# Kernel optimization log

Measured on AMD Instinct MI355X. Metric: run time of the kernel, lower is better.

## Reference

```python
import jax, jax.numpy as jnp
import numpy as np

STATE_DIM = 64
HIDDEN = 128
ACTION_DIM = 10
T = 512
B = 512


def _lstm_cell(x_t, h, c, Wi, Wh, bi, bh):
    # PyTorch LSTMCell: gates ordered (i, f, g, o)
    gates = x_t @ Wi.T + bi + h @ Wh.T + bh  # [B, 4H]
    i, f, g, o = jnp.split(gates, 4, axis=-1)
    c2 = jax.nn.sigmoid(f) * c + jax.nn.sigmoid(i) * jnp.tanh(g)
    h2 = jax.nn.sigmoid(o) * jnp.tanh(c2)
    return h2, c2


def setup_inputs() -> dict:
    key = jax.random.key(0)
    ks = jax.random.split(key, 8)
    x = jax.random.normal(ks[0], (T, B, STATE_DIM), dtype=jnp.float32)
    # LSTMCell params (PyTorch layout: weight_ih [4H, in], weight_hh [4H, H])
    s = 1.0 / np.sqrt(HIDDEN)
    W_ih0 = jax.random.uniform(ks[1], (4 * HIDDEN, STATE_DIM), minval=-s, maxval=s)
    W_hh0 = jax.random.uniform(ks[2], (4 * HIDDEN, HIDDEN), minval=-s, maxval=s)
    b_ih0 = jnp.zeros((4 * HIDDEN,), jnp.float32)
    b_hh0 = jnp.zeros((4 * HIDDEN,), jnp.float32)
    W_ih1 = jax.random.uniform(ks[3], (4 * HIDDEN, HIDDEN), minval=-s, maxval=s)
    W_hh1 = jax.random.uniform(ks[4], (4 * HIDDEN, HIDDEN), minval=-s, maxval=s)
    b_ih1 = jnp.zeros((4 * HIDDEN,), jnp.float32)
    b_hh1 = jnp.zeros((4 * HIDDEN,), jnp.float32)
    # output Linear, normc init per normc_fn
    W_out = jax.random.normal(ks[5], (ACTION_DIM, HIDDEN), dtype=jnp.float32)
    W_out = W_out / jnp.sqrt(jnp.sum(W_out ** 2, axis=1, keepdims=True))
    b_out = jnp.zeros((ACTION_DIM,), jnp.float32)
    return {"x": x, "W_ih0": W_ih0, "W_hh0": W_hh0, "b_ih0": b_ih0, "b_hh0": b_hh0,
            "W_ih1": W_ih1, "W_hh1": W_hh1, "b_ih1": b_ih1, "b_hh1": b_hh1,
            "W_out": W_out, "b_out": b_out}


def reference(x, W_ih0, W_hh0, b_ih0, b_hh0, W_ih1, W_hh1, b_ih1, b_hh1, W_out, b_out):
    # x: [T, B, state_dim]. 3D branch of LSTM_model.forward: fresh zero state,
    # two stacked LSTM cells unrolled over time, then action = tanh(Linear(h_all)).
    batch = x.shape[1]
    h0 = jnp.zeros((batch, HIDDEN), x.dtype)
    init = (h0, h0, h0, h0)  # (h_l0, c_l0, h_l1, c_l1)

    def step(carry, x_t):
        h0_, c0_, h1_, c1_ = carry
        h0n, c0n = _lstm_cell(x_t, h0_, c0_, W_ih0, W_hh0, b_ih0, b_hh0)
        h1n, c1n = _lstm_cell(h0n, h1_, c1_, W_ih1, W_hh1, b_ih1, b_hh1)
        return (h0n, c0n, h1n, c1n), h1n

    _, y = jax.lax.scan(step, init, x)  # y: [T, B, HIDDEN]
    action = jnp.tanh(y @ W_out.T + b_out)  # [T, B, action_dim]
    return action
```

## Files before the change

### kernel.cpp

```cpp
#include <hip/hip_runtime.h>
#include <stdint.h>

#define T_STEPS 512
#define B_ALL   512
#define SDIM    64
#define HID     128
#define ADIM    10
#define CB      16
#define NCH     32
#define LROW    17
#define SROW    129
#define WPAD    132

typedef __attribute__((ext_vector_type(4))) float f32x4;
typedef __attribute__((ext_vector_type(8))) short s16x8;

#define MFMA(a,b,c) __builtin_amdgcn_mfma_f32_16x16x32_bf16(a,b,c,0,0,0)
#define SC_AGENT __HIP_MEMORY_SCOPE_AGENT

__device__ __forceinline__ unsigned short bf_rne(float f){
    union{float f; unsigned int u;} v; v.f = f;
    unsigned int r = v.u + 0x7fffu + ((v.u >> 16) & 1u);
    return (unsigned short)(r >> 16);
}
__device__ __forceinline__ float us_to_f(unsigned short h){
    union{unsigned int u; float f;} v; v.u = ((unsigned int)h) << 16; return v.f;
}
__device__ __forceinline__ void split_pair(float f, unsigned short& hi, unsigned short& lo){
    hi = bf_rne(f);
    lo = bf_rne(f - us_to_f(hi));
}
__device__ __forceinline__ void load_split8(const float* p, s16x8& h, s16x8& l){
#pragma unroll
    for (int i = 0; i < 8; i++){
        unsigned short a, b; split_pair(p[i], a, b);
        h[i] = (short)a; l[i] = (short)b;
    }
}
__device__ __forceinline__ float sigm(float x){ return 1.f / (1.f + __expf(-x)); }
__device__ __forceinline__ float tanh_f(float x){ return 1.f - 2.f / (__expf(2.f * x) + 1.f); }

__device__ __forceinline__ uint32_t ep_tag(int t, int dsh){
    return (uint32_t)(((t >> dsh) + 1) & 3);
}
__device__ __forceinline__ void wait_word(const uint32_t* p, uint32_t v, uint32_t& seen){
    if (seen >= v) return;
    uint32_t c;
    while ((c = __hip_atomic_load(p, __ATOMIC_RELAXED, SC_AGENT)) < v)
        __builtin_amdgcn_s_sleep(1);
    seen = c;
    __asm__ volatile("" ::: "memory");
}
__device__ __forceinline__ int gidx(int w, int lq, int lm){ return (w * 4 + lq) * 64 + lm * 4; }

__device__ __forceinline__ void ring_load16(const float* slot, int i0, unsigned long long* pw){
#pragma unroll
    for (int g = 0; g < 4; g++){
        const unsigned long long* p = (const unsigned long long*)(slot + g * 2048 + i0);
        pw[g * 2]     = __hip_atomic_load(p,     __ATOMIC_RELAXED, SC_AGENT);
        pw[g * 2 + 1] = __hip_atomic_load(p + 1, __ATOMIC_RELAXED, SC_AGENT);
    }
}
__device__ __forceinline__ uint32_t tags_bad16(const unsigned long long* pw, uint32_t e){
    uint32_t bad = 0;
#pragma unroll
    for (int k = 0; k < 8; k++){
        uint32_t a = (uint32_t)pw[k], b = (uint32_t)(pw[k] >> 32);
        bad |= ((a ^ e) & 3u) | ((b ^ e) & 3u);
    }
    return bad;
}
__device__ __forceinline__ void pub_f4(float* dst, f32x4 v, uint32_t e){
    uint32_t q0 = (__float_as_uint(v[0]) & ~3u) | e;
    uint32_t q1 = (__float_as_uint(v[1]) & ~3u) | e;
    uint32_t q2 = (__float_as_uint(v[2]) & ~3u) | e;
    uint32_t q3 = (__float_as_uint(v[3]) & ~3u) | e;
    __hip_atomic_store((unsigned long long*)dst,
        ((unsigned long long)q1 << 32) | q0, __ATOMIC_RELAXED, SC_AGENT);
    __hip_atomic_store((unsigned long long*)dst + 1,
        ((unsigned long long)q3 << 32) | q2, __ATOMIC_RELAXED, SC_AGENT);
}

__global__ void __launch_bounds__(512, 2)
lstm_pipe(const float* __restrict__ x,
          const float* __restrict__ Wih0, const float* __restrict__ Whh0,
          const float* __restrict__ bih0, const float* __restrict__ bhh0,
          const float* __restrict__ Wih1, const float* __restrict__ Whh1,
          const float* __restrict__ bih1, const float* __restrict__ bhh1,
          const float* __restrict__ Wout, const float* __restrict__ bout,
          float* __restrict__ out, unsigned char* __restrict__ ws, int dsh)
{
    extern __shared__ uint32_t lds[];

    const int tid  = threadIdx.x;
    const int wave = tid >> 6, lane = tid & 63;
    const int lm = lane & 15, lq = lane >> 4;
    const int w  = wave;

    const int c    = blockIdx.x >> 2;
    const int role = blockIdx.x & 3;
    const int b0   = c * CB;

    const int D = 1 << dsh, dmask = D - 1;

    uint32_t* prog = (uint32_t*)(ws + (size_t)c * 512);
    unsigned char* rb = ws + 16384;
    float*    xring = (float*)rb + (size_t)c * D * 8192;
    float*    aring = (float*)(rb + (size_t)NCH * D * 32768) + (size_t)c * D * 8192;
    uint32_t* hring = (uint32_t*)(rb + (size_t)2 * NCH * D * 32768) + (size_t)c * D * 2048;

    if (role == 0){
        s16x8 wh[4][2], wl[4][2];
#pragma unroll
        for (int g = 0; g < 4; g++)
#pragma unroll
            for (int kt = 0; kt < 2; kt++){
                int j = g * HID + w * 16 + lm;
                load_split8(Wih0 + (size_t)j * SDIM + kt * 32 + lq * 8, wh[g][kt], wl[g][kt]);
            }
        uint32_t seen = 0;
        for (int t = 0; t < T_STEPS; t++){
            const float* xp = x + ((size_t)t * B_ALL + b0 + lm) * SDIM;
            s16x8 Ah[2], Al[2];
#pragma unroll
            for (int kt = 0; kt < 2; kt++)
#pragma unroll
                for (int j = 0; j < 8; j++){
                    unsigned short hh, ll; split_pair(xp[kt * 32 + lq * 8 + j], hh, ll);
                    Ah[kt][j] = (short)hh; Al[kt][j] = (short)ll;
                }
            f32x4 acc[4];
#pragma unroll
            for (int g = 0; g < 4; g++) acc[g] = (f32x4){0.f, 0.f, 0.f, 0.f};
#pragma unroll
            for (int kt = 0; kt < 2; kt++)
#pragma unroll
                for (int g = 0; g < 4; g++){
                    acc[g] = MFMA(Ah[kt], wh[g][kt], acc[g]);
                    acc[g] = MFMA(Ah[kt], wl[g][kt], acc[g]);
                    acc[g] = MFMA(Al[kt], wh[g][kt], acc[g]);
                }
            if (t >= D) wait_word(prog + 0, (uint32_t)(t - (D - 1)), seen);
            float* slot = xring + (size_t)(t & dmask) * 8192;
            uint32_t e = ep_tag(t, dsh);
#pragma unroll
            for (int g = 0; g < 4; g++)
                pub_f4(slot + g * 2048 + gidx(w, lq, lm), acc[g], e);
        }
    } else if (role == 1){
        uint32_t* stage = lds;
        s16x8 wh[4][4], wl[4][4];
#pragma unroll
        for (int g = 0; g < 4; g++)
#pragma unroll
            for (int kt = 0; kt < 4; kt++){
                int j = g * HID + w * 16 + lm;
                load_split8(Wih1 + (size_t)j * HID + kt * 32 + lq * 8, wh[g][kt], wl[g][kt]);
            }
        uint32_t seenR1 = 0;
        const int srow = 2 * w + (lane >> 5);
        const int scol = (lane & 31) * 4;
        unsigned long long hw[2];
        {
            const unsigned long long* p =
                (const unsigned long long*)(hring + srow * 128 + scol);
            hw[0] = __hip_atomic_load(p,     __ATOMIC_RELAXED, SC_AGENT);
            hw[1] = __hip_atomic_load(p + 1, __ATOMIC_RELAXED, SC_AGENT);
        }
        for (int t = 0; t < T_STEPS; t++){
            if (t && w == 0 && lane == 0)
                __hip_atomic_store(prog + 32, (uint32_t)t, __ATOMIC_RELAXED, SC_AGENT);
            uint32_t e = ep_tag(t, dsh);
            const unsigned long long* p =
                (const unsigned long long*)(hring + (size_t)(t & dmask) * 2048 + srow * 128 + scol);
            for (;;){
                uint32_t bad = 0;
#pragma unroll
                for (int k = 0; k < 2; k++){
                    uint32_t a = (uint32_t)hw[k], b = (uint32_t)(hw[k] >> 32);
                    bad |= ((a ^ e) & 3u) | ((b ^ e) & 3u);
                }
                if (__all(bad == 0)) break;
                __builtin_amdgcn_s_sleep(1);
                hw[0] = __hip_atomic_load(p,     __ATOMIC_RELAXED, SC_AGENT);
                hw[1] = __hip_atomic_load(p + 1, __ATOMIC_RELAXED, SC_AGENT);
            }
            uint32_t* sb = stage + (t & 1) * 16 * SROW + srow * SROW + scol;
            sb[0] = (uint32_t)hw[0]; sb[1] = (uint32_t)(hw[0] >> 32);
            sb[2] = (uint32_t)hw[1]; sb[3] = (uint32_t)(hw[1] >> 32);
            __syncthreads();
            if (t < T_STEPS - 1){
                const unsigned long long* pn =
                    (const unsigned long long*)(hring + (size_t)((t + 1) & dmask) * 2048 + srow * 128 + scol);
                hw[0] = __hip_atomic_load(pn,     __ATOMIC_RELAXED, SC_AGENT);
                hw[1] = __hip_atomic_load(pn + 1, __ATOMIC_RELAXED, SC_AGENT);
            }
            s16x8 Ah[4], Al[4];
            const uint32_t* sr = stage + (t & 1) * 16 * SROW + lm * SROW;
#pragma unroll
            for (int kt = 0; kt < 4; kt++)
#pragma unroll
                for (int j = 0; j < 8; j++){
                    uint32_t v = sr[kt * 32 + lq * 8 + j];
                    Ah[kt][j] = (short)(v >> 16); Al[kt][j] = (short)(v & 0xffffu);
                }
            f32x4 acc[4];
#pragma unroll
            for (int g = 0; g < 4; g++) acc[g] = (f32x4){0.f, 0.f, 0.f, 0.f};
#pragma unroll
            for (int kt = 0; kt < 4; kt++)
#pragma unroll
                for (int g = 0; g < 4; g++){
                    acc[g] = MFMA(Ah[kt], wh[g][kt], acc[g]);
                    acc[g] = MFMA(Ah[kt], wl[g][kt], acc[g]);
                    acc[g] = MFMA(Al[kt], wh[g][kt], acc[g]);
                }
            if (t >= D) wait_word(prog + 64, (uint32_t)(t - (D - 1)), seenR1);
            float* slot = aring + (size_t)(t & dmask) * 8192;
#pragma unroll
            for (int g = 0; g < 4; g++)
                pub_f4(slot + g * 2048 + gidx(w, lq, lm), acc[g], e);
        }
    } else {
        const bool isR1 = (role == 3);
        uint32_t* hbuf = lds;
        uint32_t* wlds = lds + 2 * 128 * LROW;
        for (int i = tid; i < 2 * 128 * LROW; i += 512) hbuf[i] = 0;
        if (isR1){
            for (int i = tid; i < 16 * 128; i += 512){
                int rrow = i >> 7, k = i & 127;
                uint32_t pk = 0;
                if (rrow < ADIM){
                    unsigned short hh, ll;
                    split_pair(Wout[(size_t)rrow * HID + k], hh, ll);
                    pk = ((uint32_t)hh << 16) | (uint32_t)ll;
                }
                wlds[rrow * WPAD + k] = pk;
            }
        }
        __syncthreads();

        s16x8 wh[4][4], wl[4][4];
        const float* Whh = isR1 ? Whh1 : Whh0;
#pragma unroll
        for (int g = 0; g < 4; g++)
#pragma unroll
            for (int kt = 0; kt < 4; kt++){
                int j = g * HID + w * 16 + lm;
                load_split8(Whh + (size_t)j * HID + kt * 32 + lq * 8, wh[g][kt], wl[g][kt]);
            }
        float bias[4];
#pragma unroll
        for (int g = 0; g < 4; g++){
            int j = g * HID + w * 16 + lm;
            bias[g] = isR1 ? (bih1[j] + bhh1[j]) : (bih0[j] + bhh0[j]);
        }
        float cst[4] = {0.f, 0.f, 0.f, 0.f};
        float ob = (isR1 && lm < ADIM) ? bout[lm] : 0.f;

        const float* inring = isR1 ? aring : xring;
        uint32_t* myprog    = isR1 ? (prog + 64) : (prog + 0);
        uint32_t seenBP = 0;
        const int i0 = gidx(w, lq, lm);

        unsigned long long pw[8];
        ring_load16(inring, i0, pw);

        for (int t = 0; t < T_STEPS; t++){
            if (t && w == 0 && lane == 0)
                __hip_atomic_store(myprog, (uint32_t)t, __ATOMIC_RELAXED, SC_AGENT);
            uint32_t e = ep_tag(t, dsh);
            const float* slot = inring + (size_t)(t & dmask) * 8192;
            for (;;){
                if (__all(tags_bad16(pw, e) == 0)) break;
                __builtin_amdgcn_s_sleep(1);
                ring_load16(slot, i0, pw);
            }
            f32x4 acc[4];
#pragma unroll
            for (int g = 0; g < 4; g++){
                acc[g][0] = __uint_as_float((uint32_t)pw[g * 2])             + bias[g];
                acc[g][1] = __uint_as_float((uint32_t)(pw[g * 2] >> 32))     + bias[g];
                acc[g][2] = __uint_as_float((uint32_t)pw[g * 2 + 1])         + bias[g];
                acc[g][3] = __uint_as_float((uint32_t)(pw[g * 2 + 1] >> 32)) + bias[g];
            }
            if (t < T_STEPS - 1)
                ring_load16(inring + (size_t)((t + 1) & dmask) * 8192, i0, pw);

            s16x8 Ah[4], Al[4];
            const uint32_t* hb = hbuf + ((t & 1) ^ 1) * 128 * LROW;
#pragma unroll
            for (int kt = 0; kt < 4; kt++)
#pragma unroll
                for (int j = 0; j < 8; j++){
                    uint32_t v = hb[(kt * 32 + lq * 8 + j) * LROW + lm];
                    Ah[kt][j] = (short)(v >> 16); Al[kt][j] = (short)(v & 0xffffu);
                }

            if (isR1 && t > 0 && w == (t & 7)){
                f32x4 oacc = (f32x4){0.f, 0.f, 0.f, 0.f};
#pragma unroll
                for (int kt = 0; kt < 4; kt++){
                    s16x8 oh, ol;
#pragma unroll
                    for (int j = 0; j < 8; j++){
                        uint32_t v = wlds[lm * WPAD + kt * 32 + lq * 8 + j];
                        oh[j] = (short)(v >> 16); ol[j] = (short)(v & 0xffffu);
                    }
                    oacc = MFMA(Ah[kt], oh, oacc);
                    oacc = MFMA(Ah[kt], ol, oacc);
                    oacc = MFMA(Al[kt], oh, oacc);
                }
                if (lm < ADIM){
#pragma unroll
                    for (int r = 0; r < 4; r++)
                        out[((size_t)(t - 1) * B_ALL + b0 + lq * 4 + r) * ADIM + lm] =
                            tanh_f(oacc[r] + ob);
                }
            }

#pragma unroll
            for (int kt = 0; kt < 4; kt++)
#pragma unroll
                for (int g = 0; g < 4; g++){
                    acc[g] = MFMA(Ah[kt], wh[g][kt], acc[g]);
                    acc[g] = MFMA(Ah[kt], wl[g][kt], acc[g]);
                    acc[g] = MFMA(Al[kt], wh[g][kt], acc[g]);
                }

            if (!isR1 && t >= D)
                wait_word(prog + 32, (uint32_t)(t - (D - 1)), seenBP);

            uint32_t* lb = hbuf + (t & 1) * 128 * LROW + (w * 16 + lm) * LROW + lq * 4;
            uint32_t* hdst = hring + (size_t)(t & dmask) * 2048;
#pragma unroll
            for (int r = 0; r < 4; r++){
                float zi = acc[0][r], zf = acc[1][r], zg = acc[2][r], zo = acc[3][r];
                float cn = sigm(zf) * cst[r] + sigm(zi) * tanh_f(zg);
                float hn = sigm(zo) * tanh_f(cn);
                cst[r] = cn;
                unsigned short hh, ll; split_pair(hn, hh, ll);
                lb[r] = ((uint32_t)hh << 16) | (uint32_t)ll;
                if (!isR1)
                    __hip_atomic_store(hdst + (size_t)(lq * 4 + r) * 128 + w * 16 + lm,
                                       ((uint32_t)hh << 16) | ((uint32_t)(ll & 0xfffcu)) | e,
                                       __ATOMIC_RELAXED, SC_AGENT);
            }
            __syncthreads();
        }
        if (isR1 && w == 0){
            s16x8 Ah[4], Al[4];
            const uint32_t* hb = hbuf + ((T_STEPS - 1) & 1) * 128 * LROW;
#pragma unroll
            for (int kt = 0; kt < 4; kt++)
#pragma unroll
                for (int j = 0; j < 8; j++){
                    uint32_t v = hb[(kt * 32 + lq * 8 + j) * LROW + lm];
                    Ah[kt][j] = (short)(v >> 16); Al[kt][j] = (short)(v & 0xffffu);
                }
            f32x4 oacc = (f32x4){0.f, 0.f, 0.f, 0.f};
#pragma unroll
            for (int kt = 0; kt < 4; kt++){
                s16x8 oh, ol;
#pragma unroll
                for (int j = 0; j < 8; j++){
                    uint32_t v = wlds[lm * WPAD + kt * 32 + lq * 8 + j];
                    oh[j] = (short)(v >> 16); ol[j] = (short)(v & 0xffffu);
                }
                oacc = MFMA(Ah[kt], oh, oacc);
                oacc = MFMA(Ah[kt], ol, oacc);
                oacc = MFMA(Al[kt], oh, oacc);
            }
            if (lm < ADIM){
#pragma unroll
                for (int r = 0; r < 4; r++)
                    out[((size_t)(T_STEPS - 1) * B_ALL + b0 + lq * 4 + r) * ADIM + lm] =
                        tanh_f(oacc[r] + ob);
            }
        }
    }
}

extern "C" void kernel_launch(void* const* d_in, const int* in_sizes, int n_in,
                              void* d_out, int out_size, void* d_ws, size_t ws_size,
                              hipStream_t stream)
{
    (void)in_sizes; (void)n_in; (void)out_size;
    const float* x    = (const float*)d_in[0];
    const float* Wih0 = (const float*)d_in[1];
    const float* Whh0 = (const float*)d_in[2];
    const float* bih0 = (const float*)d_in[3];
    const float* bhh0 = (const float*)d_in[4];
    const float* Wih1 = (const float*)d_in[5];
    const float* Whh1 = (const float*)d_in[6];
    const float* bih1 = (const float*)d_in[7];
    const float* bhh1 = (const float*)d_in[8];
    const float* Wout = (const float*)d_in[9];
    const float* bout = (const float*)d_in[10];

    auto need = [](int dsh){ size_t D = (size_t)1 << dsh;
                             return (size_t)16384 + (size_t)NCH * D * (2 * 32768 + 8192); };
    int dsh = 2;
    if (ws_size && ws_size < need(2)) dsh = 1;
    if (ws_size && ws_size < need(1)) dsh = 0;
    hipMemsetAsync(d_ws, 0, need(dsh), stream);

    const size_t lds_bytes = (2 * 128 * LROW + 16 * WPAD) * sizeof(uint32_t);
    hipLaunchKernelGGL(lstm_pipe, dim3(NCH * 4), dim3(512), lds_bytes, stream,
                       x, Wih0, Whh0, bih0, bhh0, Wih1, Whh1, bih1, bhh1, Wout, bout,
                       (float*)d_out, (unsigned char*)d_ws, dsh);
}
```

Measured before the change: 1.634 ms.

## Merge layer-0 input projection into recurrence block, use three-role pipeline

The layer-0 input projection (x·Wih0) is folded into the layer-0 recurrent block, so each batch chunk now runs three cooperating blocks instead of four and the x ring buffer is gone. The layer-1 input-projection block now reads h0 straight from the global ring into registers instead of staging it through LDS, and the ring depth is raised by default. This removes one cross-block handoff and its polling latency from the pipeline. In exchange, the x projection now sits on layer 0's serial critical path, which could lengthen each recurrent step.

```diff
diff --git a/kernel.cpp b/kernel.cpp
--- a/kernel.cpp
+++ b/kernel.cpp
@@ -9,8 +9,7 @@
 #define CB      16
 #define NCH     32
 #define LROW    17
-#define SROW    129
-#define WPAD    132
+#define WPAD    133
 
 typedef __attribute__((ext_vector_type(4))) float f32x4;
 typedef __attribute__((ext_vector_type(8))) short s16x8;
@@ -82,13 +81,13 @@
 }
 
 __global__ void __launch_bounds__(512, 2)
-lstm_pipe(const float* __restrict__ x,
-          const float* __restrict__ Wih0, const float* __restrict__ Whh0,
-          const float* __restrict__ bih0, const float* __restrict__ bhh0,
-          const float* __restrict__ Wih1, const float* __restrict__ Whh1,
-          const float* __restrict__ bih1, const float* __restrict__ bhh1,
-          const float* __restrict__ Wout, const float* __restrict__ bout,
-          float* __restrict__ out, unsigned char* __restrict__ ws, int dsh)
+lstm_pipe3(const float* __restrict__ x,
+           const float* __restrict__ Wih0, const float* __restrict__ Whh0,
+           const float* __restrict__ bih0, const float* __restrict__ bhh0,
+           const float* __restrict__ Wih1, const float* __restrict__ Whh1,
+           const float* __restrict__ bih1, const float* __restrict__ bhh1,
+           const float* __restrict__ Wout, const float* __restrict__ bout,
+           float* __restrict__ out, unsigned char* __restrict__ ws, int dsh)
 {
     extern __shared__ uint32_t lds[];
 
@@ -97,180 +96,217 @@
     const int lm = lane & 15, lq = lane >> 4;
     const int w  = wave;
 
-    const int c    = blockIdx.x >> 2;
-    const int role = blockIdx.x & 3;
+    const int c    = blockIdx.x / 3;
+    const int role = blockIdx.x - c * 3;
     const int b0   = c * CB;
 
     const int D = 1 << dsh, dmask = D - 1;
 
     uint32_t* prog = (uint32_t*)(ws + (size_t)c * 512);
     unsigned char* rb = ws + 16384;
-    float*    xring = (float*)rb + (size_t)c * D * 8192;
-    float*    aring = (float*)(rb + (size_t)NCH * D * 32768) + (size_t)c * D * 8192;
-    uint32_t* hring = (uint32_t*)(rb + (size_t)2 * NCH * D * 32768) + (size_t)c * D * 2048;
+    float*    aring = (float*)rb + (size_t)c * D * 8192;
+    uint32_t* hring = (uint32_t*)(rb + (size_t)NCH * D * 32768) + (size_t)c * D * 2048;
 
     if (role == 0){
-        s16x8 wh[4][2], wl[4][2];
+        uint32_t* hbuf = lds;
+        for (int i = tid; i < 2 * 128 * LROW; i += 512) hbuf[i] = 0;
+        __syncthreads();
+
+        s16x8 xh[4][2], xl[4][2];
 #pragma unroll
         for (int g = 0; g < 4; g++)
 #pragma unroll
             for (int kt = 0; kt < 2; kt++){
                 int j = g * HID + w * 16 + lm;
-                load_split8(Wih0 + (size_t)j * SDIM + kt * 32 + lq * 8, wh[g][kt], wl[g][kt]);
-            }
-        uint32_t seen = 0;
+                load_split8(Wih0 + (size_t)j * SDIM + kt * 32 + lq * 8, xh[g][kt], xl[g][kt]);
+            }
+        s16x8 wh[4][4], wl[4][4];
+#pragma unroll
+        for (int g = 0; g < 4; g++)
+#pragma unroll
+            for (int kt = 0; kt < 4; kt++){
+                int j = g * HID + w * 16 + lm;
+                load_split8(Whh0 + (size_t)j * HID + kt * 32 + lq * 8, wh[g][kt], wl[g][kt]);
+            }
+        float bias[4];
+#pragma unroll
+        for (int g = 0; g < 4; g++){
+            int j = g * HID + w * 16 + lm;
+            bias[g] = bih0[j] + bhh0[j];
+        }
+        float cst[4] = {0.f, 0.f, 0.f, 0.f};
+        uint32_t seenA = 0;
+
         for (int t = 0; t < T_STEPS; t++){
-            const float* xp = x + ((size_t)t * B_ALL + b0 + lm) * SDIM;
-            s16x8 Ah[2], Al[2];
-#pragma unroll
-            for (int kt = 0; kt < 2; kt++)
-#pragma unroll
-                for (int j = 0; j < 8; j++){
-                    unsigned short hh, ll; split_pair(xp[kt * 32 + lq * 8 + j], hh, ll);
-                    Ah[kt][j] = (short)hh; Al[kt][j] = (short)ll;
-                }
+            uint32_t e = ep_tag(t, dsh);
             f32x4 acc[4];
 #pragma unroll
+            for (int g = 0; g < 4; g++)
+                acc[g] = (f32x4){bias[g], bias[g], bias[g], bias[g]};
+            {
+                const float* xp = x + ((size_t)t * B_ALL + b0 + lm) * SDIM;
+                s16x8 Ah[2], Al[2];
+#pragma unroll
+                for (int kt = 0; kt < 2; kt++)
+#pragma unroll
+                    for (int j = 0; j < 8; j++){
+                        unsigned short hh, ll; split_pair(xp[kt * 32 + lq * 8 + j], hh, ll);
+                        Ah[kt][j] = (short)hh; Al[kt][j] = (short)ll;
+                    }
+#pragma unroll
+                for (int kt = 0; kt < 2; kt++)
+#pragma unroll
+                    for (int g = 0; g < 4; g++){
+                        acc[g] = MFMA(Ah[kt], xh[g][kt], acc[g]);
+                        acc[g] = MFMA(Ah[kt], xl[g][kt], acc[g]);
+                        acc[g] = MFMA(Al[kt], xh[g][kt], acc[g]);
+                    }
+            }
+            {
+                s16x8 Ah[4], Al[4];
+                const uint32_t* hb = hbuf + ((t & 1) ^ 1) * 128 * LROW;
+#pragma unroll
+                for (int kt = 0; kt < 4; kt++)
+#pragma unroll
+                    for (int j = 0; j < 8; j++){
+                        uint32_t v = hb[(kt * 32 + lq * 8 + j) * LROW + lm];
+                        Ah[kt][j] = (short)(v >> 16); Al[kt][j] = (short)(v & 0xffffu);
+                    }
+#pragma unroll
+                for (int kt = 0; kt < 4; kt++)
+#pragma unroll
+                    for (int g = 0; g < 4; g++){
+                        acc[g] = MFMA(Ah[kt], wh[g][kt], acc[g]);
+                        acc[g] = MFMA(Ah[kt], wl[g][kt], acc[g]);
+                        acc[g] = MFMA(Al[kt], wh[g][kt], acc[g]);
+                    }
+            }
+            if (t >= D) wait_word(prog + 32, (uint32_t)(t - (D - 1)), seenA);
+
+            uint32_t* lb = hbuf + (t & 1) * 128 * LROW + (w * 16 + lm) * LROW + lq * 4;
+            uint32_t* hdst = hring + (size_t)(t & dmask) * 2048;
+#pragma unroll
+            for (int r = 0; r < 4; r++){
+                float zi = acc[0][r], zf = acc[1][r], zg = acc[2][r], zo = acc[3][r];
+                float cn = sigm(zf) * cst[r] + sigm(zi) * tanh_f(zg);
+                float hn = sigm(zo) * tanh_f(cn);
+                cst[r] = cn;
+                unsigned short hh, ll; split_pair(hn, hh, ll);
+                lb[r] = ((uint32_t)hh << 16) | (uint32_t)ll;
+                __hip_atomic_store(hdst + (size_t)(lq * 4 + r) * 128 + w * 16 + lm,
+                                   ((uint32_t)hh << 16) | ((uint32_t)(ll & 0xfffcu)) | e,
+                                   __ATOMIC_RELAXED, SC_AGENT);
+            }
+            __syncthreads();
+        }
+    } else if (role == 1){
+        s16x8 wh[4][4], wl[4][4];
+#pragma unroll
+        for (int g = 0; g < 4; g++)
+#pragma unroll
+            for (int kt = 0; kt < 4; kt++){
+                int j = g * HID + w * 16 + lm;
+                load_split8(Wih1 + (size_t)j * HID + kt * 32 + lq * 8, wh[g][kt], wl[g][kt]);
+            }
+        uint32_t seenR1 = 0;
+        const int hbase = lm * 64 + lq * 4;
+        unsigned long long hw[16];
+        auto hload = [&](const uint32_t* slot){
+            const unsigned long long* p = (const unsigned long long*)slot + hbase;
+#pragma unroll
+            for (int kt = 0; kt < 4; kt++)
+#pragma unroll
+                for (int q = 0; q < 4; q++)
+                    hw[kt * 4 + q] = __hip_atomic_load(p + kt * 16 + q, __ATOMIC_RELAXED, SC_AGENT);
+        };
+        hload(hring);
+        for (int t = 0; t < T_STEPS; t++){
+            __syncthreads();
+            if (t && w == 0 && lane == 0)
+                __hip_atomic_store(prog + 32, (uint32_t)t, __ATOMIC_RELAXED, SC_AGENT);
+            uint32_t e = ep_tag(t, dsh);
+            const uint32_t* slot = hring + (size_t)(t & dmask) * 2048;
+            for (;;){
+                uint32_t bad = 0;
+#pragma unroll
+                for (int k = 0; k < 16; k++){
+                    uint32_t a = (uint32_t)hw[k], b = (uint32_t)(hw[k] >> 32);
+                    bad |= ((a ^ e) & 3u) | ((b ^ e) & 3u);
+                }
+                if (__all(bad == 0)) break;
+                __builtin_amdgcn_s_sleep(1);
+                hload(slot);
+            }
+            s16x8 Ah[4], Al[4];
+#pragma unroll
+            for (int kt = 0; kt < 4; kt++)
+#pragma unroll
+                for (int q = 0; q < 4; q++){
+                    uint32_t a = (uint32_t)hw[kt * 4 + q], b = (uint32_t)(hw[kt * 4 + q] >> 32);
+                    Ah[kt][2*q]   = (short)(a >> 16); Al[kt][2*q]   = (short)(a & 0xffffu);
+                    Ah[kt][2*q+1] = (short)(b >> 16); Al[kt][2*q+1] = (short)(b & 0xffffu);
+                }
+            if (t < T_STEPS - 1)
+                hload(hring + (size_t)((t + 1) & dmask) * 2048);
+            f32x4 acc[4];
+#pragma unroll
             for (int g = 0; g < 4; g++) acc[g] = (f32x4){0.f, 0.f, 0.f, 0.f};
 #pragma unroll
-            for (int kt = 0; kt < 2; kt++)
+            for (int kt = 0; kt < 4; kt++)
 #pragma unroll
                 for (int g = 0; g < 4; g++){
                     acc[g] = MFMA(Ah[kt], wh[g][kt], acc[g]);
                     acc[g] = MFMA(Ah[kt], wl[g][kt], acc[g]);
                     acc[g] = MFMA(Al[kt], wh[g][kt], acc[g]);
                 }
-            if (t >= D) wait_word(prog + 0, (uint32_t)(t - (D - 1)), seen);
-            float* slot = xring + (size_t)(t & dmask) * 8192;
-            uint32_t e = ep_tag(t, dsh);
+            if (t >= D) wait_word(prog + 64, (uint32_t)(t - (D - 1)), seenR1);
+            float* slotw = aring + (size_t)(t & dmask) * 8192;
 #pragma unroll
             for (int g = 0; g < 4; g++)
-                pub_f4(slot + g * 2048 + gidx(w, lq, lm), acc[g], e);
-        }
-    } else if (role == 1){
-        uint32_t* stage = lds;
-        s16x8 wh[4][4], wl[4][4];
-#pragma unroll
-        for (int g = 0; g < 4; g++)
-#pragma unroll
-            for (int kt = 0; kt < 4; kt++){
-                int j = g * HID + w * 16 + lm;
-                load_split8(Wih1 + (size_t)j * HID + kt * 32 + lq * 8, wh[g][kt], wl[g][kt]);
-            }
-        uint32_t seenR1 = 0;
-        const int srow = 2 * w + (lane >> 5);
-        const int scol = (lane & 31) * 4;
-        unsigned long long hw[2];
-        {
-            const unsigned long long* p =
-                (const unsigned long long*)(hring + srow * 128 + scol);
-            hw[0] = __hip_atomic_load(p,     __ATOMIC_RELAXED, SC_AGENT);
-            hw[1] = __hip_atomic_load(p + 1, __ATOMIC_RELAXED, SC_AGENT);
-        }
-        for (int t = 0; t < T_STEPS; t++){
-            if (t && w == 0 && lane == 0)
-                __hip_atomic_store(prog + 32, (uint32_t)t, __ATOMIC_RELAXED, SC_AGENT);
-            uint32_t e = ep_tag(t, dsh);
-            const unsigned long long* p =
-                (const unsigned long long*)(hring + (size_t)(t & dmask) * 2048 + srow * 128 + scol);
-            for (;;){
-                uint32_t bad = 0;
-#pragma unroll
-                for (int k = 0; k < 2; k++){
-                    uint32_t a = (uint32_t)hw[k], b = (uint32_t)(hw[k] >> 32);
-                    bad |= ((a ^ e) & 3u) | ((b ^ e) & 3u);
-                }
-                if (__all(bad == 0)) break;
-                __builtin_amdgcn_s_sleep(1);
-                hw[0] = __hip_atomic_load(p,     __ATOMIC_RELAXED, SC_AGENT);
-                hw[1] = __hip_atomic_load(p + 1, __ATOMIC_RELAXED, SC_AGENT);
-            }
-            uint32_t* sb = stage + (t & 1) * 16 * SROW + srow * SROW + scol;
-            sb[0] = (uint32_t)hw[0]; sb[1] = (uint32_t)(hw[0] >> 32);
-            sb[2] = (uint32_t)hw[1]; sb[3] = (uint32_t)(hw[1] >> 32);
-            __syncthreads();
-            if (t < T_STEPS - 1){
-                const unsigned long long* pn =
-                    (const unsigned long long*)(hring + (size_t)((t + 1) & dmask) * 2048 + srow * 128 + scol);
-                hw[0] = __hip_atomic_load(pn,     __ATOMIC_RELAXED, SC_AGENT);
-                hw[1] = __hip_atomic_load(pn + 1, __ATOMIC_RELAXED, SC_AGENT);
-            }
-            s16x8 Ah[4], Al[4];
-            const uint32_t* sr = stage + (t & 1) * 16 * SROW + lm * SROW;
-#pragma unroll
-            for (int kt = 0; kt < 4; kt++)
-#pragma unroll
-                for (int j = 0; j < 8; j++){
-                    uint32_t v = sr[kt * 32 + lq * 8 + j];
-                    Ah[kt][j] = (short)(v >> 16); Al[kt][j] = (short)(v & 0xffffu);
-                }
-            f32x4 acc[4];
-#pragma unroll
-            for (int g = 0; g < 4; g++) acc[g] = (f32x4){0.f, 0.f, 0.f, 0.f};
-#pragma unroll
-            for (int kt = 0; kt < 4; kt++)
-#pragma unroll
-                for (int g = 0; g < 4; g++){
-                    acc[g] = MFMA(Ah[kt], wh[g][kt], acc[g]);
-                    acc[g] = MFMA(Ah[kt], wl[g][kt], acc[g]);
-                    acc[g] = MFMA(Al[kt], wh[g][kt], acc[g]);
-                }
-            if (t >= D) wait_word(prog + 64, (uint32_t)(t - (D - 1)), seenR1);
-            float* slot = aring + (size_t)(t & dmask) * 8192;
-#pragma unroll
-            for (int g = 0; g < 4; g++)
-                pub_f4(slot + g * 2048 + gidx(w, lq, lm), acc[g], e);
+                pub_f4(slotw + g * 2048 + gidx(w, lq, lm), acc[g], e);
         }
     } else {
-        const bool isR1 = (role == 3);
         uint32_t* hbuf = lds;
         uint32_t* wlds = lds + 2 * 128 * LROW;
         for (int i = tid; i < 2 * 128 * LROW; i += 512) hbuf[i] = 0;
-        if (isR1){
-            for (int i = tid; i < 16 * 128; i += 512){
-                int rrow = i >> 7, k = i & 127;
-                uint32_t pk = 0;
-                if (rrow < ADIM){
-                    unsigned short hh, ll;
-                    split_pair(Wout[(size_t)rrow * HID + k], hh, ll);
-                    pk = ((uint32_t)hh << 16) | (uint32_t)ll;
-                }
-                wlds[rrow * WPAD + k] = pk;
-            }
+        for (int i = tid; i < 16 * 128; i += 512){
+            int rrow = i >> 7, k = i & 127;
+            uint32_t pk = 0;
+            if (rrow < ADIM){
+                unsigned short hh, ll;
+                split_pair(Wout[(size_t)rrow * HID + k], hh, ll);
+                pk = ((uint32_t)hh << 16) | (uint32_t)ll;
+            }
+            wlds[rrow * WPAD + k] = pk;
         }
         __syncthreads();
 
         s16x8 wh[4][4], wl[4][4];
-        const float* Whh = isR1 ? Whh1 : Whh0;
 #pragma unroll
         for (int g = 0; g < 4; g++)
 #pragma unroll
             for (int kt = 0; kt < 4; kt++){
                 int j = g * HID + w * 16 + lm;
-                load_split8(Whh + (size_t)j * HID + kt * 32 + lq * 8, wh[g][kt], wl[g][kt]);
+                load_split8(Whh1 + (size_t)j * HID + kt * 32 + lq * 8, wh[g][kt], wl[g][kt]);
             }
         float bias[4];
 #pragma unroll
         for (int g = 0; g < 4; g++){
             int j = g * HID + w * 16 + lm;
-            bias[g] = isR1 ? (bih1[j] + bhh1[j]) : (bih0[j] + bhh0[j]);
+            bias[g] = bih1[j] + bhh1[j];
         }
         float cst[4] = {0.f, 0.f, 0.f, 0.f};
-        float ob = (isR1 && lm < ADIM) ? bout[lm] : 0.f;
-
-        const float* inring = isR1 ? aring : xring;
-        uint32_t* myprog    = isR1 ? (prog + 64) : (prog + 0);
-        uint32_t seenBP = 0;
+        float ob = (lm < ADIM) ? bout[lm] : 0.f;
         const int i0 = gidx(w, lq, lm);
 
         unsigned long long pw[8];
-        ring_load16(inring, i0, pw);
+        ring_load16(aring, i0, pw);
 
         for (int t = 0; t < T_STEPS; t++){
             if (t && w == 0 && lane == 0)
-                __hip_atomic_store(myprog, (uint32_t)t, __ATOMIC_RELAXED, SC_AGENT);
+                __hip_atomic_store(prog + 64, (uint32_t)t, __ATOMIC_RELAXED, SC_AGENT);
             uint32_t e = ep_tag(t, dsh);
-            const float* slot = inring + (size_t)(t & dmask) * 8192;
+            const float* slot = aring + (size_t)(t & dmask) * 8192;
             for (;;){
                 if (__all(tags_bad16(pw, e) == 0)) break;
                 __builtin_amdgcn_s_sleep(1);
@@ -285,7 +321,7 @@
                 acc[g][3] = __uint_as_float((uint32_t)(pw[g * 2 + 1] >> 32)) + bias[g];
             }
             if (t < T_STEPS - 1)
-                ring_load16(inring + (size_t)((t + 1) & dmask) * 8192, i0, pw);
+                ring_load16(aring + (size_t)((t + 1) & dmask) * 8192, i0, pw);
 
             s16x8 Ah[4], Al[4];
             const uint32_t* hb = hbuf + ((t & 1) ^ 1) * 128 * LROW;
@@ -297,7 +333,7 @@
                     Ah[kt][j] = (short)(v >> 16); Al[kt][j] = (short)(v & 0xffffu);
                 }
 
-            if (isR1 && t > 0 && w == (t & 7)){
+            if (t > 0 && w == (t & 7)){
                 f32x4 oacc = (f32x4){0.f, 0.f, 0.f, 0.f};
 #pragma unroll
                 for (int kt = 0; kt < 4; kt++){
@@ -328,11 +364,7 @@
                     acc[g] = MFMA(Al[kt], wh[g][kt], acc[g]);
                 }
 
-            if (!isR1 && t >= D)
-                wait_word(prog + 32, (uint32_t)(t - (D - 1)), seenBP);
-
             uint32_t* lb = hbuf + (t & 1) * 128 * LROW + (w * 16 + lm) * LROW + lq * 4;
-            uint32_t* hdst = hring + (size_t)(t & dmask) * 2048;
 #pragma unroll
             for (int r = 0; r < 4; r++){
                 float zi = acc[0][r], zf = acc[1][r], zg = acc[2][r], zo = acc[3][r];
@@ -341,14 +373,10 @@
                 cst[r] = cn;
                 unsigned short hh, ll; split_pair(hn, hh, ll);
                 lb[r] = ((uint32_t)hh << 16) | (uint32_t)ll;
-                if (!isR1)
-                    __hip_atomic_store(hdst + (size_t)(lq * 4 + r) * 128 + w * 16 + lm,
-                                       ((uint32_t)hh << 16) | ((uint32_t)(ll & 0xfffcu)) | e,
-                                       __ATOMIC_RELAXED, SC_AGENT);
             }
             __syncthreads();
         }
-        if (isR1 && w == 0){
+        if (w == 0){
             s16x8 Ah[4], Al[4];
             const uint32_t* hb = hbuf + ((T_STEPS - 1) & 1) * 128 * LROW;
 #pragma unroll
@@ -399,14 +427,13 @@
     const float* bout = (const float*)d_in[10];
 
     auto need = [](int dsh){ size_t D = (size_t)1 << dsh;
-                             return (size_t)16384 + (size_t)NCH * D * (2 * 32768 + 8192); };
-    int dsh = 2;
-    if (ws_size && ws_size < need(2)) dsh = 1;
-    if (ws_size && ws_size < need(1)) dsh = 0;
+                             return (size_t)16384 + (size_t)NCH * D * (32768 + 8192); };
+    int dsh = 3;
+    while (dsh > 0 && ws_size && ws_size < need(dsh)) dsh--;
     hipMemsetAsync(d_ws, 0, need(dsh), stream);
 
     const size_t lds_bytes = (2 * 128 * LROW + 16 * WPAD) * sizeof(uint32_t);
-    hipLaunchKernelGGL(lstm_pipe, dim3(NCH * 4), dim3(512), lds_bytes, stream,
+    hipLaunchKernelGGL(lstm_pipe3, dim3(NCH * 3), dim3(512), lds_bytes, stream,
                        x, Wih0, Whh0, bih0, bhh0, Wih1, Whh1, bih1, bhh1, Wout, bout,
                        (float*)d_out, (unsigned char*)d_ws, dsh);
 }
```

Result: slower. 2.585 ms (+58.2%).
